# Performance work log

Hardware: AMD Instinct MI355X
Metric: run time of the kernel (lower is better)

Reference implementation:

```python
import jax, jax.numpy as jnp
import numpy as np

DIM = 1024
VOCAB = 32000
NSEQ = 32
LENGTHS = 64 - np.arange(NSEQ) // 2  # descending seq lengths 64..49 (packed seqs are length-sorted)


def setup_inputs() -> dict:
    key = jax.random.key(0)
    k1, k2, k3, k4, k5 = jax.random.split(key, 5)
    T = int(LENGTHS.max())
    batch_sizes = np.array([(LENGTHS > t).sum() for t in range(T)], dtype=np.int32)
    total = int(batch_sizes.sum())  # 1808 packed tokens
    hidden_states = jax.random.normal(k1, (total, 2 * DIM), dtype=jnp.float32)
    sentences = jax.random.randint(k2, (total,), 0, VOCAB, dtype=jnp.int32)
    weight = jax.random.normal(k3, (VOCAB, DIM), dtype=jnp.float32) * (1.0 / np.sqrt(DIM))
    fwd_bias = jax.random.normal(k4, (VOCAB,), dtype=jnp.float32) * 0.01
    bwd_bias = jax.random.normal(k5, (VOCAB,), dtype=jnp.float32) * 0.01
    return {
        "hidden_states": hidden_states,
        "weight": weight,
        "fwd_bias": fwd_bias,
        "bwd_bias": bwd_bias,
        "sentences": sentences,
        "batch_sizes": jnp.asarray(batch_sizes),
    }


def _build_indices(batch_sizes):
    # Static (host-side) index construction replicating the per-timestep Python loops.
    bs = np.asarray(batch_sizes)
    off = np.concatenate([[0], np.cumsum(bs)])  # start row of each timestep block
    T = len(bs)
    # forward: hidden at t-1 (first bs[t] rows) predicts token at t
    ctx_f = np.concatenate([off[t - 1] + np.arange(bs[t]) for t in range(1, T)])
    tgt_f = np.concatenate([off[t] + np.arange(bs[t]) for t in range(1, T)])
    # backward: hidden at i+1 predicts token at i (first bs[i+1] rows), i = T-2 .. 1
    ctx_b = np.concatenate([off[i + 1] + np.arange(bs[i + 1]) for i in range(1, T - 1)])
    tgt_b = np.concatenate([off[i] + np.arange(bs[i + 1]) for i in range(1, T - 1)])
    denom = float(2 * bs.sum() - bs[0] - bs[-1])
    return ctx_f, tgt_f, ctx_b, tgt_b, denom


def _ce_sum(h, W, b, tgt):
    # sum-reduced cross entropy: one fused GEMM over all packed rows
    logits = h @ W.T + b  # [N, V]
    lse = jax.nn.logsumexp(logits, axis=-1)  # [N]
    gold = jnp.take_along_axis(logits, tgt[:, None], axis=1)[:, 0]  # [N]
    return jnp.sum(lse - gold)


def reference(hidden_states, weight, fwd_bias, bwd_bias, sentences, batch_sizes):
    dim = hidden_states.shape[1] // 2
    ctx_f, tgt_f, ctx_b, tgt_b, denom = _build_indices(batch_sizes)
    loss_f = _ce_sum(hidden_states[ctx_f, :dim], weight, fwd_bias, sentences[tgt_f])
    loss_b = _ce_sum(hidden_states[ctx_b, dim:], weight, bwd_bias, sentences[tgt_b])
    return (loss_f + loss_b) / denom
```

## Files before the change

kernel.cpp:

```cpp
#include <hip/hip_runtime.h>
#include <hip/hip_bf16.h>
#include <stdint.h>

typedef float f32x16 __attribute__((ext_vector_type(16)));
typedef int   i32x4  __attribute__((ext_vector_type(4)));
typedef int   i32x8  __attribute__((ext_vector_type(8)));

#define LOG2E 1.4426950408889634f
#define WSCALE 16.0f


__device__ __forceinline__ uint32_t f32_to_e4m3(float x) {
    uint32_t ux = __float_as_uint(x);
    uint32_t s = (ux >> 24) & 0x80u;
    float a = __uint_as_float(ux & 0x7FFFFFFFu);
    if (a >= 448.0f) return s | 0x7Eu;
    int e = (int)((ux >> 23) & 0xFFu) - 127;
    if (e < -6) {
        int n = __float2int_rn(a * 512.0f);
        return s | (uint32_t)n;
    }
    uint32_t m = ux & 0x7FFFFFu;
    uint32_t r = (m + 0x7FFFFu + ((m >> 20) & 1u)) >> 20;
    if (r == 8u) { r = 0u; e += 1; }
    if (e > 8 || (e == 8 && r == 7u)) return s | 0x7Eu;
    return s | ((uint32_t)(e + 7) << 3) | r;
}

__device__ __forceinline__ uint32_t pack4_fp8v(float4 v, float sc) {
    return f32_to_e4m3(v.x * sc) | (f32_to_e4m3(v.y * sc) << 8) |
           (f32_to_e4m3(v.z * sc) << 16) | (f32_to_e4m3(v.w * sc) << 24);
}

__device__ __forceinline__ uint32_t pack4_fp8(const float* s, float sc) {
    return f32_to_e4m3(s[0] * sc) | (f32_to_e4m3(s[1] * sc) << 8) |
           (f32_to_e4m3(s[2] * sc) << 16) | (f32_to_e4m3(s[3] * sc) << 24);
}

__device__ __forceinline__ uint4 cvt16_fp8(const float* s, float sc) {
    uint4 r;
    r.x = pack4_fp8(s, sc);      r.y = pack4_fp8(s + 4, sc);
    r.z = pack4_fp8(s + 8, sc);  r.w = pack4_fp8(s + 12, sc);
    return r;
}

__global__ void prep_kernel(const int* __restrict__ bs, int T,
                            const int* __restrict__ sentences,
                            int* __restrict__ hdr, float* __restrict__ fhdr,
                            int* __restrict__ row_ctx, int* __restrict__ row_tok) {
    __shared__ int off[1025];
    if (threadIdx.x == 0) {
        int acc = 0; off[0] = 0;
        for (int t = 0; t < T; ++t) { acc += bs[t]; off[t + 1] = acc; }
    }
    __syncthreads();
    const int total = off[T];
    const int Nf = total - off[1];
    const int Nb = total - off[2];
    for (int t = 1; t < T; ++t) {
        int start = off[t] - off[1];
        int cnt = off[t + 1] - off[t];
        for (int p = threadIdx.x; p < cnt; p += blockDim.x) {
            row_ctx[start + p] = off[t - 1] + p;
            row_tok[start + p] = sentences[off[t] + p];
        }
    }
    for (int i = 1; i < T - 1; ++i) {
        int start = Nf + off[i + 1] - off[2];
        int cnt = off[i + 2] - off[i + 1];
        for (int p = threadIdx.x; p < cnt; p += blockDim.x) {
            row_ctx[start + p] = off[i + 1] + p;
            row_tok[start + p] = sentences[off[i] + p];
        }
    }
    if (threadIdx.x == 0) {
        hdr[0] = Nf + Nb;
        hdr[1] = Nf;
        int bs0 = off[1];
        int bsl = off[T] - off[T - 1];
        fhdr[0] = (float)(2 * total - bs0 - bsl);
    }
}

__global__ void wconv_kernel(const float* __restrict__ W,
                             uint8_t* __restrict__ Wb, int K) {
    const int p = blockIdx.x >> 3, f = blockIdx.x & 7;
    __shared__ __align__(16) char tile[2048];
    char* panel = (char*)Wb + (size_t)p * ((size_t)K << 8);
    const int tid = threadIdx.x;
    const int rloc = tid >> 4;
    const int kloc = (tid & 15) << 2;
    const int h = (kloc >> 4) & 1;
    const int l = ((kloc >> 5) << 5) | rloc;
    const int ldst = h * 1024 + l * 16 + (kloc & 15);
    const float* src = W + (size_t)(p * 256 + f * 32 + rloc) * K + kloc;
    const int NT = K >> 6;
    for (int t = 0; t < NT; ++t) {
        const float4 v = *(const float4*)(src + t * 64);
        const uint32_t pk = pack4_fp8v(v, WSCALE);
        __syncthreads();
        *(uint32_t*)(tile + ldst) = pk;
        __syncthreads();
        if (tid < 128)
            *(uint4*)(panel + (size_t)t * 16384 + f * 2048 + (tid << 4)) =
                *(const uint4*)(tile + (tid << 4));
    }
}

__global__ void gather_kernel(const float* __restrict__ hs,
                              const int* __restrict__ row_ctx,
                              const int* __restrict__ hdr,
                              uint8_t* __restrict__ Hc,
                              float* __restrict__ S, int D2, int K) {
    const int p = blockIdx.x >> 2, f = blockIdx.x & 3;
    const int M = hdr[0], Nf = hdr[1];
    if (f == 0 && threadIdx.x < 128) S[p * 128 + threadIdx.x] = 0.f;
    char* panel = (char*)Hc + (size_t)p * ((size_t)K << 7);
    const int row0 = p * 128 + f * 32;
    const int nch = (K >> 6) << 7;
    for (int c = threadIdx.x; c < nch; c += 512) {
        const int t = c >> 7, h = (c >> 6) & 1, l = c & 63;
        const int row = row0 + (l & 31);
        char* d = panel + (size_t)t * 8192 + f * 2048 + h * 1024 + l * 16;
        if (row >= M) {
            uint4 z; z.x = z.y = z.z = z.w = 0u;
            *(uint4*)d = z;
        } else {
            const int ctx = row_ctx[row];
            const int k = t * 64 + ((l >> 5) << 5) + h * 16;
            *(uint4*)d = cvt16_fp8(hs + (size_t)ctx * D2 + (row < Nf ? 0 : K) + k, 1.0f);
        }
    }
}

__global__ __launch_bounds__(256, 3)
void gemm_lse(const uint8_t* __restrict__ A,
              const uint8_t* __restrict__ B,
              const float* __restrict__ fb,
              const float* __restrict__ bb,
              float* __restrict__ S,
              const int* __restrict__ hdr, int K, int MT) {
    const int M = hdr[0], Nf = hdr[1];

    const int nwg = gridDim.x, orig = blockIdx.x;
    const int q = nwg >> 3, rr = nwg & 7;
    const int xcd = orig & 7, i8 = orig >> 3;
    const int wgid = (xcd < rr ? xcd * (q + 1) : rr * (q + 1) + (xcd - rr) * q) + i8;
    const int bm = wgid % MT, bn = wgid / MT;
    if (bm * 128 >= M) return;

    const int tid = threadIdx.x, lane = tid & 63, wid = tid >> 6;
    const int wm = wid >> 1, wn = wid & 1;

    f32x16 acc00 = (f32x16)0.f, acc01 = (f32x16)0.f;
    f32x16 acc10 = (f32x16)0.f, acc11 = (f32x16)0.f;

    const char* pa = (const char*)A + (size_t)bm * ((size_t)K << 7)
                     + (wm << 12) + (lane << 4);
    const char* pb = (const char*)B + (size_t)(bn >> 1) * ((size_t)K << 8)
                     + ((bn & 1) << 13) + (wn << 12) + (lane << 4);

    i32x4 xa0l, xa0h, xa1l, xa1h, xb0l, xb0h, xb1l, xb1h;
    i32x4 ya0l, ya0h, ya1l, ya1h, yb0l, yb0h, yb1l, yb1h;

#define LOADS(P, t) do {                                                      \
    const char* _a = pa + (size_t)(t) * 8192;                                 \
    const char* _b = pb + (size_t)(t) * 16384;                                \
    P##a0l = *(const i32x4*)(_a);          P##a0h = *(const i32x4*)(_a + 1024); \
    P##a1l = *(const i32x4*)(_a + 2048);   P##a1h = *(const i32x4*)(_a + 3072); \
    P##b0l = *(const i32x4*)(_b);          P##b0h = *(const i32x4*)(_b + 1024); \
    P##b1l = *(const i32x4*)(_b + 2048);   P##b1h = *(const i32x4*)(_b + 3072); \
} while (0)

#define CAT8(lo, hi) __builtin_shufflevector(lo, hi, 0, 1, 2, 3, 4, 5, 6, 7)

#define COMP(P) do {                                                          \
    const i32x8 A0 = CAT8(P##a0l, P##a0h);                                    \
    const i32x8 A1 = CAT8(P##a1l, P##a1h);                                    \
    const i32x8 B0 = CAT8(P##b0l, P##b0h);                                    \
    const i32x8 B1 = CAT8(P##b1l, P##b1h);                                    \
    acc00 = __builtin_amdgcn_mfma_scale_f32_32x32x64_f8f6f4(                  \
        A0, B0, acc00, 0, 0, 0, 127, 0, 127);                                 \
    acc01 = __builtin_amdgcn_mfma_scale_f32_32x32x64_f8f6f4(                  \
        A0, B1, acc01, 0, 0, 0, 127, 0, 127);                                 \
    acc10 = __builtin_amdgcn_mfma_scale_f32_32x32x64_f8f6f4(                  \
        A1, B0, acc10, 0, 0, 0, 127, 0, 127);                                 \
    acc11 = __builtin_amdgcn_mfma_scale_f32_32x32x64_f8f6f4(                  \
        A1, B1, acc11, 0, 0, 0, 127, 0, 127);                                 \
} while (0)

    const int NT = K >> 6;

    LOADS(x, 0);
    int t = 0;
    for (; t + 2 < NT; t += 2) {
        LOADS(y, t + 1);
        COMP(x);
        LOADS(x, t + 2);
        COMP(y);
    }
    if ((NT & 1) == 0) {
        LOADS(y, t + 1);
        COMP(x);
        COMP(y);
    } else {
        COMP(x);
    }

    const float k1 = LOG2E / WSCALE;
    const int v0 = bn * 128 + wn * 64 + (lane & 31);
    const float fbv0 = fb[v0] * LOG2E,      bbv0 = bb[v0] * LOG2E;
    const float fbv1 = fb[v0 + 32] * LOG2E, bbv1 = bb[v0 + 32] * LOG2E;
    const int mb0 = bm * 128 + wm * 64 + ((lane >> 5) << 2);

#define EPI(T0, T1, MB) do {                                                  \
    _Pragma("unroll")                                                         \
    for (int reg = 0; reg < 16; ++reg) {                                      \
        const int m = (MB) + (reg & 3) + ((reg >> 2) << 3);                   \
        if (m < M) {           \
            const bool isf = m < Nf;                                          \
            float ps = exp2f(fmaf(T0[reg], k1, isf ? fbv0 : bbv0))            \
                     + exp2f(fmaf(T1[reg], k1, isf ? fbv1 : bbv1));           \
            _Pragma("unroll")                                                 \
            for (int s = 1; s < 32; s <<= 1) ps += __shfl_xor(ps, s);         \
            if ((lane & 31) == 0) atomicAdd(&S[m], ps);                       \
        }                                                                     \
    }                                                                         \
} while (0)

    EPI(acc00, acc01, mb0);
    EPI(acc10, acc11, mb0 + 32);

#undef LOADS
#undef CAT8
#undef COMP
#undef EPI
}

__global__ void lse_naive(const float* __restrict__ hs,
                          const float* __restrict__ W,
                          const float* __restrict__ fb,
                          const float* __restrict__ bb,
                          const int* __restrict__ row_ctx,
                          const int* __restrict__ hdr,
                          float* __restrict__ S, int D2, int D, int V) {
    const int m = blockIdx.x;
    const int M = hdr[0], Nf = hdr[1];
    if (m >= M) return;
    __shared__ float hrow[2048];
    const int ctx = row_ctx[m];
    const float* h = hs + (size_t)ctx * D2 + (m < Nf ? 0 : D);
    for (int i = threadIdx.x; i < D; i += blockDim.x) hrow[i] = h[i];
    __syncthreads();
    const float* bias = (m < Nf) ? fb : bb;
    float ps = 0.f;
    for (int v = threadIdx.x; v < V; v += blockDim.x) {
        const float* w = W + (size_t)v * D;
        float dot = 0.f;
        for (int k = 0; k < D; ++k) dot = fmaf(hrow[k], w[k], dot);
        ps += exp2f((dot + bias[v]) * LOG2E);
    }
#pragma unroll
    for (int d = 1; d < 64; d <<= 1) ps += __shfl_xor(ps, d);
    __shared__ float wsum[4];
    const int wid = threadIdx.x >> 6, lane = threadIdx.x & 63;
    if (lane == 0) wsum[wid] = ps;
    __syncthreads();
    if (threadIdx.x == 0) S[m] = wsum[0] + wsum[1] + wsum[2] + wsum[3];
}

__global__ void gold_kernel(const float* __restrict__ hs,
                            const float* __restrict__ W,
                            const float* __restrict__ fb,
                            const float* __restrict__ bb,
                            const int* __restrict__ row_ctx,
                            const int* __restrict__ row_tok,
                            const int* __restrict__ hdr,
                            float* __restrict__ goldv, int D2, int D) {
    const int m = blockIdx.x;
    const int M = hdr[0];
    if (m >= M) return;
    const int Nf = hdr[1];
    const int ctx = row_ctx[m], tok = row_tok[m];
    const float4* h = (const float4*)(hs + (size_t)ctx * D2 + (m < Nf ? 0 : D));
    const float4* w = (const float4*)(W + (size_t)tok * D);
    float s = 0.f;
    for (int i = threadIdx.x; i < D / 4; i += blockDim.x) {
        float4 a = h[i], b = w[i];
        s += a.x * b.x + a.y * b.y + a.z * b.z + a.w * b.w;
    }
#pragma unroll
    for (int d = 1; d < 64; d <<= 1) s += __shfl_xor(s, d);
    __shared__ float wsum[4];
    const int wid = threadIdx.x >> 6, lane = threadIdx.x & 63;
    if (lane == 0) wsum[wid] = s;
    __syncthreads();
    if (threadIdx.x == 0) {
        float tot = wsum[0] + wsum[1] + wsum[2] + wsum[3];
        tot += (m < Nf ? fb[tok] : bb[tok]);
        goldv[m] = tot;
    }
}

__global__ void final_kernel(const float* __restrict__ S,
                             const float* __restrict__ goldv,
                             const int* __restrict__ hdr,
                             const float* __restrict__ fhdr,
                             float* __restrict__ out) {
    const int M = hdr[0];
    float s = 0.f;
    for (int m = threadIdx.x; m < M; m += blockDim.x)
        s += logf(S[m]) - goldv[m];
#pragma unroll
    for (int d = 1; d < 64; d <<= 1) s += __shfl_xor(s, d);
    __shared__ float wsum[4];
    const int wid = threadIdx.x >> 6, lane = threadIdx.x & 63;
    if (lane == 0) wsum[wid] = s;
    __syncthreads();
    if (threadIdx.x == 0)
        out[0] = (wsum[0] + wsum[1] + wsum[2] + wsum[3]) / fhdr[0];
}

extern "C" void kernel_launch(void* const* d_in, const int* in_sizes, int n_in,
                              void* d_out, int out_size, void* d_ws, size_t ws_size,
                              hipStream_t stream) {
    const float* hs  = (const float*)d_in[0];
    const float* W   = (const float*)d_in[1];
    const float* fb  = (const float*)d_in[2];
    const float* bb  = (const float*)d_in[3];
    const int* sent  = (const int*)d_in[4];
    const int* bs    = (const int*)d_in[5];
    const int total  = in_sizes[4];
    const int T      = in_sizes[5];
    const int V      = in_sizes[2];
    const int D      = in_sizes[1] / V;
    const int D2     = in_sizes[0] / total;
    const int Mcap   = ((2 * total) + 127) & ~127;
    const int MT     = Mcap / 128;
    const int NN2    = V / 128;

    char* p = (char*)d_ws;
    int*   hdr     = (int*)p;            p += 256;
    float* fhdr    = (float*)p;          p += 256;
    int*   row_ctx = (int*)p;            p += (size_t)Mcap * 4;
    int*   row_tok = (int*)p;            p += (size_t)Mcap * 4;
    float* S       = (float*)p;          p += (size_t)Mcap * 4;
    float* goldv   = (float*)p;          p += (size_t)Mcap * 4;
    uint8_t* Hc    = (uint8_t*)p;        p += (size_t)Mcap * D;
    uint8_t* Wb    = (uint8_t*)p;
    const size_t need_wb = (size_t)(p - (char*)d_ws) + (size_t)V * D;

    prep_kernel<<<1, 256, 0, stream>>>(bs, T, sent, hdr, fhdr, row_ctx, row_tok);

    if (ws_size >= need_wb) {
        gather_kernel<<<MT * 4, 512, 0, stream>>>(hs, row_ctx, hdr, Hc, S, D2, D);
        wconv_kernel<<<(V / 256) * 8, 512, 0, stream>>>(W, Wb, D);
        gemm_lse<<<NN2 * MT, 256, 0, stream>>>(Hc, Wb, fb, bb, S, hdr, D, MT);
    } else {
        lse_naive<<<Mcap, 256, 0, stream>>>(hs, W, fb, bb, row_ctx, hdr, S, D2, D, V);
    }

    gold_kernel<<<Mcap, 256, 0, stream>>>(hs, W, fb, bb, row_ctx, row_tok, hdr, goldv, D2, D);
    final_kernel<<<1, 256, 0, stream>>>(S, goldv, hdr, fhdr, (float*)d_out);
}
```

Before: 283.5 us.

## Compute each 128x128 GEMM tile with a single wave holding 4x4 accumulators

```diff
diff --git a/kernel.cpp b/kernel.cpp
--- a/kernel.cpp
+++ b/kernel.cpp
@@ -133,7 +133,7 @@
     }
 }
 
-__global__ __launch_bounds__(256, 3)
+__global__ __launch_bounds__(64, 1)
 void gemm_lse(const uint8_t* __restrict__ A,
               const uint8_t* __restrict__ B,
               const float* __restrict__ fb,
@@ -149,44 +149,46 @@
     const int bm = wgid % MT, bn = wgid / MT;
     if (bm * 128 >= M) return;
 
-    const int tid = threadIdx.x, lane = tid & 63, wid = tid >> 6;
-    const int wm = wid >> 1, wn = wid & 1;
-
-    f32x16 acc00 = (f32x16)0.f, acc01 = (f32x16)0.f;
-    f32x16 acc10 = (f32x16)0.f, acc11 = (f32x16)0.f;
+    const int lane = threadIdx.x;
+
+    f32x16 acc[4][4];
+#pragma unroll
+    for (int i = 0; i < 4; ++i)
+#pragma unroll
+        for (int j = 0; j < 4; ++j) acc[i][j] = (f32x16)0.f;
 
     const char* pa = (const char*)A + (size_t)bm * ((size_t)K << 7)
-                     + (wm << 12) + (lane << 4);
+                     + (lane << 4);
     const char* pb = (const char*)B + (size_t)(bn >> 1) * ((size_t)K << 8)
-                     + ((bn & 1) << 13) + (wn << 12) + (lane << 4);
-
-    i32x4 xa0l, xa0h, xa1l, xa1h, xb0l, xb0h, xb1l, xb1h;
-    i32x4 ya0l, ya0h, ya1l, ya1h, yb0l, yb0h, yb1l, yb1h;
+                     + ((bn & 1) << 13) + (lane << 4);
+
+    i32x4 x[16], y[16];
 
 #define LOADS(P, t) do {                                                      \
     const char* _a = pa + (size_t)(t) * 8192;                                 \
     const char* _b = pb + (size_t)(t) * 16384;                                \
-    P##a0l = *(const i32x4*)(_a);          P##a0h = *(const i32x4*)(_a + 1024); \
-    P##a1l = *(const i32x4*)(_a + 2048);   P##a1h = *(const i32x4*)(_a + 3072); \
-    P##b0l = *(const i32x4*)(_b);          P##b0h = *(const i32x4*)(_b + 1024); \
-    P##b1l = *(const i32x4*)(_b + 2048);   P##b1h = *(const i32x4*)(_b + 3072); \
+    _Pragma("unroll")                                                         \
+    for (int _f = 0; _f < 4; ++_f) {                                          \
+        P[2 * _f]     = *(const i32x4*)(_a + _f * 2048);                      \
+        P[2 * _f + 1] = *(const i32x4*)(_a + _f * 2048 + 1024);               \
+        P[8 + 2 * _f]     = *(const i32x4*)(_b + _f * 2048);                  \
+        P[8 + 2 * _f + 1] = *(const i32x4*)(_b + _f * 2048 + 1024);           \
+    }                                                                         \
 } while (0)
 
 #define CAT8(lo, hi) __builtin_shufflevector(lo, hi, 0, 1, 2, 3, 4, 5, 6, 7)
 
 #define COMP(P) do {                                                          \
-    const i32x8 A0 = CAT8(P##a0l, P##a0h);                                    \
-    const i32x8 A1 = CAT8(P##a1l, P##a1h);                                    \
-    const i32x8 B0 = CAT8(P##b0l, P##b0h);                                    \
-    const i32x8 B1 = CAT8(P##b1l, P##b1h);                                    \
-    acc00 = __builtin_amdgcn_mfma_scale_f32_32x32x64_f8f6f4(                  \
-        A0, B0, acc00, 0, 0, 0, 127, 0, 127);                                 \
-    acc01 = __builtin_amdgcn_mfma_scale_f32_32x32x64_f8f6f4(                  \
-        A0, B1, acc01, 0, 0, 0, 127, 0, 127);                                 \
-    acc10 = __builtin_amdgcn_mfma_scale_f32_32x32x64_f8f6f4(                  \
-        A1, B0, acc10, 0, 0, 0, 127, 0, 127);                                 \
-    acc11 = __builtin_amdgcn_mfma_scale_f32_32x32x64_f8f6f4(                  \
-        A1, B1, acc11, 0, 0, 0, 127, 0, 127);                                 \
+    _Pragma("unroll")                                                         \
+    for (int _f = 0; _f < 4; ++_f) {                                          \
+        const i32x8 _A = CAT8(P[2 * _f], P[2 * _f + 1]);                      \
+        _Pragma("unroll")                                                     \
+        for (int _g = 0; _g < 4; ++_g) {                                      \
+            const i32x8 _B = CAT8(P[8 + 2 * _g], P[8 + 2 * _g + 1]);          \
+            acc[_f][_g] = __builtin_amdgcn_mfma_scale_f32_32x32x64_f8f6f4(    \
+                _A, _B, acc[_f][_g], 0, 0, 0, 127, 0, 127);                   \
+        }                                                                     \
+    }                                                                         \
 } while (0)
 
     const int NT = K >> 6;
@@ -208,33 +210,35 @@
     }
 
     const float k1 = LOG2E / WSCALE;
-    const int v0 = bn * 128 + wn * 64 + (lane & 31);
-    const float fbv0 = fb[v0] * LOG2E,      bbv0 = bb[v0] * LOG2E;
-    const float fbv1 = fb[v0 + 32] * LOG2E, bbv1 = bb[v0 + 32] * LOG2E;
-    const int mb0 = bm * 128 + wm * 64 + ((lane >> 5) << 2);
-
-#define EPI(T0, T1, MB) do {                                                  \
-    _Pragma("unroll")                                                         \
-    for (int reg = 0; reg < 16; ++reg) {                                      \
-        const int m = (MB) + (reg & 3) + ((reg >> 2) << 3);                   \
-        if (m < M) {           \
-            const bool isf = m < Nf;                                          \
-            float ps = exp2f(fmaf(T0[reg], k1, isf ? fbv0 : bbv0))            \
-                     + exp2f(fmaf(T1[reg], k1, isf ? fbv1 : bbv1));           \
-            _Pragma("unroll")                                                 \
-            for (int s = 1; s < 32; s <<= 1) ps += __shfl_xor(ps, s);         \
-            if ((lane & 31) == 0) atomicAdd(&S[m], ps);                       \
-        }                                                                     \
-    }                                                                         \
-} while (0)
-
-    EPI(acc00, acc01, mb0);
-    EPI(acc10, acc11, mb0 + 32);
-
+    const int v0 = bn * 128 + (lane & 31);
+    float fbv[4], bbv[4];
+#pragma unroll
+    for (int g = 0; g < 4; ++g) {
+        fbv[g] = fb[v0 + g * 32] * LOG2E;
+        bbv[g] = bb[v0 + g * 32] * LOG2E;
+    }
+    const int mb0 = bm * 128 + ((lane >> 5) << 2);
+
+#pragma unroll
+    for (int f = 0; f < 4; ++f) {
+#pragma unroll
+        for (int reg = 0; reg < 16; ++reg) {
+            const int m = mb0 + f * 32 + (reg & 3) + ((reg >> 2) << 3);
+            if (m < M) {
+                const bool isf = m < Nf;
+                float ps = 0.f;
+#pragma unroll
+                for (int g = 0; g < 4; ++g)
+                    ps += exp2f(fmaf(acc[f][g][reg], k1, isf ? fbv[g] : bbv[g]));
+#pragma unroll
+                for (int s = 1; s < 32; s <<= 1) ps += __shfl_xor(ps, s);
+                if ((lane & 31) == 0) atomicAdd(&S[m], ps);
+            }
+        }
+    }
 #undef LOADS
 #undef CAT8
 #undef COMP
-#undef EPI
 }
 
 __global__ void lse_naive(const float* __restrict__ hs,
@@ -355,7 +359,7 @@
     if (ws_size >= need_wb) {
         gather_kernel<<<MT * 4, 512, 0, stream>>>(hs, row_ctx, hdr, Hc, S, D2, D);
         wconv_kernel<<<(V / 256) * 8, 512, 0, stream>>>(W, Wb, D);
-        gemm_lse<<<NN2 * MT, 256, 0, stream>>>(Hc, Wb, fb, bb, S, hdr, D, MT);
+        gemm_lse<<<NN2 * MT, 64, 0, stream>>>(Hc, Wb, fb, bb, S, hdr, D, MT);
     } else {
         lse_naive<<<Mcap, 256, 0, stream>>>(hs, W, fb, bb, row_ctx, hdr, S, D2, D, V);
     }
```

Result: slower. 387.7 us (+36.8%).

## Fuse weight conversion, gather and gold-logit kernels into one staging launch

Applied to the files above, without the earlier changes.

```diff
diff --git a/kernel.cpp b/kernel.cpp
--- a/kernel.cpp
+++ b/kernel.cpp
@@ -82,58 +82,86 @@
     }
 }
 
-__global__ void wconv_kernel(const float* __restrict__ W,
-                             uint8_t* __restrict__ Wb, int K) {
-    const int p = blockIdx.x >> 3, f = blockIdx.x & 7;
-    __shared__ __align__(16) char tile[2048];
-    char* panel = (char*)Wb + (size_t)p * ((size_t)K << 8);
+__global__ void stage_all(const float* __restrict__ W,
+                          const float* __restrict__ hs,
+                          const int* __restrict__ row_ctx,
+                          const int* __restrict__ row_tok,
+                          const int* __restrict__ hdr,
+                          const float* __restrict__ fb,
+                          const float* __restrict__ bb,
+                          uint8_t* __restrict__ Wb,
+                          uint8_t* __restrict__ Hc,
+                          float* __restrict__ S,
+                          float* __restrict__ goldv,
+                          int K, int D2, int NWC, int NGA) {
+    const int bx = blockIdx.x;
     const int tid = threadIdx.x;
-    const int rloc = tid >> 4;
-    const int kloc = (tid & 15) << 2;
-    const int h = (kloc >> 4) & 1;
-    const int l = ((kloc >> 5) << 5) | rloc;
-    const int ldst = h * 1024 + l * 16 + (kloc & 15);
-    const float* src = W + (size_t)(p * 256 + f * 32 + rloc) * K + kloc;
-    const int NT = K >> 6;
-    for (int t = 0; t < NT; ++t) {
-        const float4 v = *(const float4*)(src + t * 64);
-        const uint32_t pk = pack4_fp8v(v, WSCALE);
-        __syncthreads();
-        *(uint32_t*)(tile + ldst) = pk;
-        __syncthreads();
-        if (tid < 128)
-            *(uint4*)(panel + (size_t)t * 16384 + f * 2048 + (tid << 4)) =
-                *(const uint4*)(tile + (tid << 4));
-    }
-}
-
-__global__ void gather_kernel(const float* __restrict__ hs,
-                              const int* __restrict__ row_ctx,
-                              const int* __restrict__ hdr,
-                              uint8_t* __restrict__ Hc,
-                              float* __restrict__ S, int D2, int K) {
-    const int p = blockIdx.x >> 2, f = blockIdx.x & 3;
+    if (bx < NWC) {
+        const int p = bx >> 3, f = bx & 7;
+        __shared__ __align__(16) char tile[2048];
+        char* panel = (char*)Wb + (size_t)p * ((size_t)K << 8);
+        const int rloc = tid >> 4;
+        const int kloc = (tid & 15) << 2;
+        const int h = (kloc >> 4) & 1;
+        const int l = ((kloc >> 5) << 5) | rloc;
+        const int ldst = h * 1024 + l * 16 + (kloc & 15);
+        const float* src = W + (size_t)(p * 256 + f * 32 + rloc) * K + kloc;
+        const int NT = K >> 6;
+        for (int t = 0; t < NT; ++t) {
+            const float4 v = *(const float4*)(src + t * 64);
+            const uint32_t pk = pack4_fp8v(v, WSCALE);
+            __syncthreads();
+            *(uint32_t*)(tile + ldst) = pk;
+            __syncthreads();
+            if (tid < 128)
+                *(uint4*)(panel + (size_t)t * 16384 + f * 2048 + (tid << 4)) =
+                    *(const uint4*)(tile + (tid << 4));
+        }
+        return;
+    }
     const int M = hdr[0], Nf = hdr[1];
-    if (f == 0 && threadIdx.x < 128) S[p * 128 + threadIdx.x] = 0.f;
-    char* panel = (char*)Hc + (size_t)p * ((size_t)K << 7);
-    const int row0 = p * 128 + f * 32;
-    const int nch = (K >> 6) << 7;
-    for (int c = threadIdx.x; c < nch; c += 512) {
-        const int t = c >> 7, h = (c >> 6) & 1, l = c & 63;
-        const int row = row0 + (l & 31);
-        char* d = panel + (size_t)t * 8192 + f * 2048 + h * 1024 + l * 16;
-        if (row >= M) {
-            uint4 z; z.x = z.y = z.z = z.w = 0u;
-            *(uint4*)d = z;
-        } else {
-            const int ctx = row_ctx[row];
-            const int k = t * 64 + ((l >> 5) << 5) + h * 16;
-            *(uint4*)d = cvt16_fp8(hs + (size_t)ctx * D2 + (row < Nf ? 0 : K) + k, 1.0f);
+    if (bx < NWC + NGA) {
+        const int bx2 = bx - NWC;
+        const int p = bx2 >> 2, f = bx2 & 3;
+        if (f == 0 && tid < 128) S[p * 128 + tid] = 0.f;
+        char* panel = (char*)Hc + (size_t)p * ((size_t)K << 7);
+        const int row0 = p * 128 + f * 32;
+        const int nch = (K >> 6) << 7;
+        for (int c = tid; c < nch; c += 512) {
+            const int t = c >> 7, h = (c >> 6) & 1, l = c & 63;
+            const int row = row0 + (l & 31);
+            char* d = panel + (size_t)t * 8192 + f * 2048 + h * 1024 + l * 16;
+            if (row >= M) {
+                uint4 z; z.x = z.y = z.z = z.w = 0u;
+                *(uint4*)d = z;
+            } else {
+                const int ctx = row_ctx[row];
+                const int k = t * 64 + ((l >> 5) << 5) + h * 16;
+                *(uint4*)d = cvt16_fp8(hs + (size_t)ctx * D2 + (row < Nf ? 0 : K) + k, 1.0f);
+            }
         }
-    }
-}
-
-__global__ __launch_bounds__(256, 3)
+        return;
+    }
+    const int bx3 = bx - NWC - NGA;
+    const int lane = tid & 63, wid = tid >> 6;
+    const int m = (bx3 << 3) + wid;
+    if (m >= M) return;
+    const int ctx = row_ctx[m], tok = row_tok[m];
+    const float4* h = (const float4*)(hs + (size_t)ctx * D2 + (m < Nf ? 0 : K));
+    const float4* w = (const float4*)(W + (size_t)tok * K);
+    float s = 0.f;
+#pragma unroll
+    for (int j = 0; j < 4; ++j) {
+        const int i = lane + j * 64;
+        float4 a = h[i], b = w[i];
+        s += a.x * b.x + a.y * b.y + a.z * b.z + a.w * b.w;
+    }
+#pragma unroll
+    for (int d = 1; d < 64; d <<= 1) s += __shfl_xor(s, d);
+    if (lane == 0) goldv[m] = s + (m < Nf ? fb[tok] : bb[tok]);
+}
+
+__global__ __launch_bounds__(256, 4)
 void gemm_lse(const uint8_t* __restrict__ A,
               const uint8_t* __restrict__ B,
               const float* __restrict__ fb,
@@ -149,7 +177,7 @@
     const int bm = wgid % MT, bn = wgid / MT;
     if (bm * 128 >= M) return;
 
-    const int tid = threadIdx.x, lane = tid & 63, wid = tid >> 6;
+    const int lane = threadIdx.x & 63, wid = threadIdx.x >> 6;
     const int wm = wid >> 1, wn = wid & 1;
 
     f32x16 acc00 = (f32x16)0.f, acc01 = (f32x16)0.f;
@@ -160,51 +188,33 @@
     const char* pb = (const char*)B + (size_t)(bn >> 1) * ((size_t)K << 8)
                      + ((bn & 1) << 13) + (wn << 12) + (lane << 4);
 
-    i32x4 xa0l, xa0h, xa1l, xa1h, xb0l, xb0h, xb1l, xb1h;
-    i32x4 ya0l, ya0h, ya1l, ya1h, yb0l, yb0h, yb1l, yb1h;
-
-#define LOADS(P, t) do {                                                      \
-    const char* _a = pa + (size_t)(t) * 8192;                                 \
-    const char* _b = pb + (size_t)(t) * 16384;                                \
-    P##a0l = *(const i32x4*)(_a);          P##a0h = *(const i32x4*)(_a + 1024); \
-    P##a1l = *(const i32x4*)(_a + 2048);   P##a1h = *(const i32x4*)(_a + 3072); \
-    P##b0l = *(const i32x4*)(_b);          P##b0h = *(const i32x4*)(_b + 1024); \
-    P##b1l = *(const i32x4*)(_b + 2048);   P##b1h = *(const i32x4*)(_b + 3072); \
-} while (0)
-
 #define CAT8(lo, hi) __builtin_shufflevector(lo, hi, 0, 1, 2, 3, 4, 5, 6, 7)
 
-#define COMP(P) do {                                                          \
-    const i32x8 A0 = CAT8(P##a0l, P##a0h);                                    \
-    const i32x8 A1 = CAT8(P##a1l, P##a1h);                                    \
-    const i32x8 B0 = CAT8(P##b0l, P##b0h);                                    \
-    const i32x8 B1 = CAT8(P##b1l, P##b1h);                                    \
-    acc00 = __builtin_amdgcn_mfma_scale_f32_32x32x64_f8f6f4(                  \
-        A0, B0, acc00, 0, 0, 0, 127, 0, 127);                                 \
-    acc01 = __builtin_amdgcn_mfma_scale_f32_32x32x64_f8f6f4(                  \
-        A0, B1, acc01, 0, 0, 0, 127, 0, 127);                                 \
-    acc10 = __builtin_amdgcn_mfma_scale_f32_32x32x64_f8f6f4(                  \
-        A1, B0, acc10, 0, 0, 0, 127, 0, 127);                                 \
-    acc11 = __builtin_amdgcn_mfma_scale_f32_32x32x64_f8f6f4(                  \
-        A1, B1, acc11, 0, 0, 0, 127, 0, 127);                                 \
-} while (0)
-
     const int NT = K >> 6;
 
-    LOADS(x, 0);
-    int t = 0;
-    for (; t + 2 < NT; t += 2) {
-        LOADS(y, t + 1);
-        COMP(x);
-        LOADS(x, t + 2);
-        COMP(y);
-    }
-    if ((NT & 1) == 0) {
-        LOADS(y, t + 1);
-        COMP(x);
-        COMP(y);
-    } else {
-        COMP(x);
+    for (int t = 0; t < NT; ++t) {
+        const char* _a = pa + (size_t)t * 8192;
+        const char* _b = pb + (size_t)t * 16384;
+        const i32x4 a0l = *(const i32x4*)(_a);
+        const i32x4 a0h = *(const i32x4*)(_a + 1024);
+        const i32x4 a1l = *(const i32x4*)(_a + 2048);
+        const i32x4 a1h = *(const i32x4*)(_a + 3072);
+        const i32x4 b0l = *(const i32x4*)(_b);
+        const i32x4 b0h = *(const i32x4*)(_b + 1024);
+        const i32x4 b1l = *(const i32x4*)(_b + 2048);
+        const i32x4 b1h = *(const i32x4*)(_b + 3072);
+        const i32x8 A0 = CAT8(a0l, a0h);
+        const i32x8 A1 = CAT8(a1l, a1h);
+        const i32x8 B0 = CAT8(b0l, b0h);
+        const i32x8 B1 = CAT8(b1l, b1h);
+        acc00 = __builtin_amdgcn_mfma_scale_f32_32x32x64_f8f6f4(
+            A0, B0, acc00, 0, 0, 0, 127, 0, 127);
+        acc01 = __builtin_amdgcn_mfma_scale_f32_32x32x64_f8f6f4(
+            A0, B1, acc01, 0, 0, 0, 127, 0, 127);
+        acc10 = __builtin_amdgcn_mfma_scale_f32_32x32x64_f8f6f4(
+            A1, B0, acc10, 0, 0, 0, 127, 0, 127);
+        acc11 = __builtin_amdgcn_mfma_scale_f32_32x32x64_f8f6f4(
+            A1, B1, acc11, 0, 0, 0, 127, 0, 127);
     }
 
     const float k1 = LOG2E / WSCALE;
@@ -231,9 +241,7 @@
     EPI(acc00, acc01, mb0);
     EPI(acc10, acc11, mb0 + 32);
 
-#undef LOADS
 #undef CAT8
-#undef COMP
 #undef EPI
 }
 
@@ -353,13 +361,16 @@
     prep_kernel<<<1, 256, 0, stream>>>(bs, T, sent, hdr, fhdr, row_ctx, row_tok);
 
     if (ws_size >= need_wb) {
-        gather_kernel<<<MT * 4, 512, 0, stream>>>(hs, row_ctx, hdr, Hc, S, D2, D);
-        wconv_kernel<<<(V / 256) * 8, 512, 0, stream>>>(W, Wb, D);
+        const int NWC = (V / 256) * 8;
+        const int NGA = MT * 4;
+        const int NGO = Mcap / 8;
+        stage_all<<<NWC + NGA + NGO, 512, 0, stream>>>(
+            W, hs, row_ctx, row_tok, hdr, fb, bb, Wb, Hc, S, goldv, D, D2, NWC, NGA);
         gemm_lse<<<NN2 * MT, 256, 0, stream>>>(Hc, Wb, fb, bb, S, hdr, D, MT);
     } else {
         lse_naive<<<Mcap, 256, 0, stream>>>(hs, W, fb, bb, row_ctx, hdr, S, D2, D, V);
-    }
-
-    gold_kernel<<<Mcap, 256, 0, stream>>>(hs, W, fb, bb, row_ctx, row_tok, hdr, goldv, D2, D);
+        gold_kernel<<<Mcap, 256, 0, stream>>>(hs, W, fb, bb, row_ctx, row_tok, hdr, goldv, D2, D);
+    }
+
     final_kernel<<<1, 256, 0, stream>>>(S, goldv, hdr, fhdr, (float*)d_out);
 }
```

Result: faster. 257.0 us (-9.3%).
